# Kernel optimization log

Measured on AMD Instinct MI355X. Metric: run time of the kernel, lower is better.

## Reference

```python
import jax, jax.numpy as jnp
import numpy as np

B, S = 16, 8192
Q_DIM, K_DIM, ATTN_DIM = 512, 512, 512


def setup_inputs() -> dict:
    key = jax.random.key(0)
    k1, k2, k3, k4, k5, k6 = jax.random.split(key, 6)
    query = jax.random.normal(k1, (B, Q_DIM), dtype=jnp.float32)
    keys = jax.random.normal(k2, (B, S, K_DIM), dtype=jnp.float32)
    mask = jax.random.randint(k3, (B, S), 0, 2, dtype=jnp.int32)
    # learned params (torch Linear stores weight as [out, in]; we keep [in, out])
    Wq = jax.random.normal(k4, (Q_DIM, ATTN_DIM), dtype=jnp.float32) / np.sqrt(Q_DIM)
    Wk = jax.random.normal(k5, (K_DIM, ATTN_DIM), dtype=jnp.float32) / np.sqrt(K_DIM)
    v = jax.random.normal(k6, (ATTN_DIM,), dtype=jnp.float32) / np.sqrt(ATTN_DIM)
    return {"query": query, "keys": keys, "mask": mask, "Wq": Wq, "Wk": Wk, "v": v}


def reference(query, keys, mask, Wq, Wk, v):
    # q: [B, 1, A], k: [B, S, A]
    q = (query @ Wq)[:, None, :]
    k = jnp.einsum('bsk,ka->bsa', keys, Wk)
    # scores e: [B, S]  (v-projection reduces attn dim)
    e = jnp.einsum('bsa,a->bs', jnp.tanh(q + k), v)
    neg_min = jnp.finfo(e.dtype).min
    e = jnp.where(mask == 0, neg_min, e)
    a = jax.nn.softmax(e, axis=-1)  # [B, S]
    c = jnp.einsum('bs,bsk->bk', a, keys)  # context [B, K_DIM]
    return (c, a)
```

## Files before the change

### kernel.cpp

```cpp
#include <hip/hip_runtime.h>

#define BB 16
#define SS 8192
#define DD 512

typedef float  f32x4  __attribute__((ext_vector_type(4)));
typedef __bf16 bf16x8 __attribute__((ext_vector_type(8)));
typedef __bf16 bf16x4 __attribute__((ext_vector_type(4)));

__device__ __forceinline__ void gload_lds16(const unsigned short* g, unsigned short* l) {
    __builtin_amdgcn_global_load_lds(
        (const __attribute__((address_space(1))) unsigned int*)(g),
        (__attribute__((address_space(3))) unsigned int*)(l), 16, 0, 0);
}

__device__ __forceinline__ void cvt_store_bf4(unsigned short* dst, f32x4 v) {
    bf16x4 o;
    o.x = (__bf16)v.x; o.y = (__bf16)v.y; o.z = (__bf16)v.z; o.w = (__bf16)v.w;
    *(bf16x4*)dst = o;
}

__device__ __forceinline__ float tanh_fast(float x) {
    float e2 = __expf(2.0f * x);
    return 1.0f - 2.0f / (e2 + 1.0f);
}

__global__ void prep_kernel(const float* __restrict__ query, const float* __restrict__ Wq,
                            const float* __restrict__ Wk, float* __restrict__ qproj,
                            unsigned short* __restrict__ WkT)
{
    const int bid = blockIdx.x, t = threadIdx.x;
    if (bid < DD) {
        const int n = bid;
        for (int k = t; k < DD; k += 256) {
            __bf16 h = (__bf16)Wk[k * DD + n];
            WkT[n * DD + k] = __builtin_bit_cast(unsigned short, h);
        }
    } else {
        const int idx = (bid - DD) * 256 + t;
        const int b = idx >> 9;
        const int n = idx & 511;
        const float* q  = query + b * DD;
        const float* wp = Wq + n;
        float acc = 0.0f;
#pragma unroll 8
        for (int k = 0; k < DD; ++k)
            acc = fmaf(q[k], wp[(size_t)k * DD], acc);
        qproj[b * DD + n] = acc;
    }
}

__global__ __launch_bounds__(256, 2) void fused_kernel(
    const float* __restrict__ keys, const unsigned short* __restrict__ WkT,
    const float* __restrict__ qproj, const float* __restrict__ vvec,
    const int* __restrict__ mask, float* __restrict__ e_ws,
    float* __restrict__ cpart, float2* __restrict__ ml_ws)
{
    __shared__ unsigned short ksA[2][4 * 512];
    __shared__ unsigned short wtB[2][32 * 512];
    __shared__ float sm_part[4][64];
    __shared__ float w_sh[64];
    __shared__ f32x4 red[128];

    const int tid  = threadIdx.x;
    const int w    = tid >> 6;
    const int lane = tid & 63;
    const int ml   = lane & 15;
    const int quad = lane >> 4;
    const int bid  = blockIdx.x;
    const int b    = bid >> 7;
    const int chunk = bid & 127;
    const int s0   = chunk << 6;

    const int m  = tid >> 2;
    const int q4 = tid & 3;
    const float* krow = keys + ((size_t)(b * SS + s0 + m)) * DD + q4 * 4;
    const int it  = m >> 4;
    const int g0  = q4 >> 1;
    const int j0  = (q4 & 1) * 4;
    const int stA0 = it * 512 + ((m & 15) + 16 * g0)       * 8 + j0;
    const int stA1 = it * 512 + ((m & 15) + 16 * (g0 + 2)) * 8 + j0;

    const unsigned short* wg = WkT + (size_t)(w * 128 + ml) * DD + quad * 8;

    f32x4 acc[4][8];
#pragma unroll
    for (int i = 0; i < 4; ++i)
#pragma unroll
        for (int jn = 0; jn < 8; ++jn) acc[i][jn] = (f32x4){0.f, 0.f, 0.f, 0.f};

#pragma unroll
    for (int r = 0; r < 8; ++r)
        gload_lds16(wg + (size_t)r * 16 * DD, &wtB[0][(w * 8 + r) * 512]);
    {
        f32x4 k0 = *(const f32x4*)(krow);
        f32x4 k1 = *(const f32x4*)(krow + 16);
        cvt_store_bf4(&ksA[0][stA0], k0);
        cvt_store_bf4(&ksA[0][stA1], k1);
    }
    __syncthreads();

    for (int j = 0; j < 16; ++j) {
        const int cur = j & 1;
        const int nxt = cur ^ 1;
        f32x4 k0, k1;
        if (j < 15) {
            const int kb = (j + 1) * 32;
#pragma unroll
            for (int r = 0; r < 8; ++r)
                gload_lds16(wg + kb + (size_t)r * 16 * DD, &wtB[nxt][(w * 8 + r) * 512]);
            k0 = *(const f32x4*)(krow + kb);
            k1 = *(const f32x4*)(krow + kb + 16);
        }
        bf16x8 af[4];
#pragma unroll
        for (int i = 0; i < 4; ++i)
            af[i] = *(const bf16x8*)&ksA[cur][i * 512 + lane * 8];
#pragma unroll
        for (int jn = 0; jn < 8; ++jn) {
            bf16x8 bfr = *(const bf16x8*)&wtB[cur][(w * 8 + jn) * 512 + lane * 8];
#pragma unroll
            for (int i = 0; i < 4; ++i)
                acc[i][jn] = __builtin_amdgcn_mfma_f32_16x16x32_bf16(af[i], bfr, acc[i][jn], 0, 0, 0);
        }
        if (j < 15) {
            cvt_store_bf4(&ksA[nxt][stA0], k0);
            cvt_store_bf4(&ksA[nxt][stA1], k1);
        }
        __syncthreads();
    }

    float qv[8], vv[8];
#pragma unroll
    for (int jn = 0; jn < 8; ++jn) {
        const int n = w * 128 + jn * 16 + ml;
        qv[jn] = qproj[b * DD + n];
        vv[jn] = vvec[n];
    }
#pragma unroll
    for (int i = 0; i < 4; ++i) {
#pragma unroll
        for (int r = 0; r < 4; ++r) {
            float s = 0.0f;
#pragma unroll
            for (int jn = 0; jn < 8; ++jn) {
                float xx = acc[i][jn][r] + qv[jn];
                s += tanh_fast(xx) * vv[jn];
            }
            s += __shfl_xor(s, 1, 64);
            s += __shfl_xor(s, 2, 64);
            s += __shfl_xor(s, 4, 64);
            s += __shfl_xor(s, 8, 64);
            if (ml == 0) sm_part[w][i * 16 + quad * 4 + r] = s;
        }
    }
    __syncthreads();

    if (tid < 64) {
        float e = sm_part[0][tid] + sm_part[1][tid] + sm_part[2][tid] + sm_part[3][tid];
        const int mk = mask[b * SS + s0 + tid];
        if (mk == 0) e = -3.402823466e38f;
        e_ws[(size_t)b * SS + s0 + tid] = e;
        float mx = e;
#pragma unroll
        for (int off = 32; off >= 1; off >>= 1) mx = fmaxf(mx, __shfl_xor(mx, off, 64));
        float wv = (mk == 0) ? 0.0f : __expf(e - mx);
        float l  = wv;
#pragma unroll
        for (int off = 32; off >= 1; off >>= 1) l += __shfl_xor(l, off, 64);
        w_sh[tid] = wv;
        if (tid == 0) ml_ws[b * 128 + chunk] = make_float2(mx, l);
    }
    __syncthreads();

    const int n4 = (tid & 127) << 2;
    const int sh = tid >> 7;
    const float* kctx = keys + ((size_t)(b * SS + s0 + sh * 32)) * DD + n4;
    f32x4 cacc = (f32x4){0.f, 0.f, 0.f, 0.f};
#pragma unroll 8
    for (int sI = 0; sI < 32; ++sI) {
        float wgt = w_sh[sh * 32 + sI];
        f32x4 kv  = *(const f32x4*)(kctx + (size_t)sI * DD);
        cacc += kv * wgt;
    }
    if (sh == 1) red[tid & 127] = cacc;
    __syncthreads();
    if (sh == 0) {
        cacc += red[tid];
        *(f32x4*)(cpart + ((size_t)(b * 128 + chunk)) * 512 + n4) = cacc;
    }
}

__global__ __launch_bounds__(256) void finalize_kernel(
    const float* __restrict__ e_ws, const float* __restrict__ cpart,
    const float2* __restrict__ ml_ws, float* __restrict__ out)
{
    const int bid = blockIdx.x, t = threadIdx.x;
    const int b = (bid < 16) ? bid : ((bid - 16) >> 3);

    float mi = -3.402823466e38f, li = 0.0f;
    if (t < 128) { float2 p = ml_ws[b * 128 + t]; mi = p.x; li = p.y; }
    float mr = mi;
#pragma unroll
    for (int off = 32; off >= 1; off >>= 1) mr = fmaxf(mr, __shfl_xor(mr, off, 64));
    __shared__ float rm[4], rs[4];
    if ((t & 63) == 0) rm[t >> 6] = mr;
    __syncthreads();
    const float M = fmaxf(fmaxf(rm[0], rm[1]), fmaxf(rm[2], rm[3]));
    float si = (t < 128) ? li * __expf(mi - M) : 0.0f;
#pragma unroll
    for (int off = 32; off >= 1; off >>= 1) si += __shfl_xor(si, off, 64);
    if ((t & 63) == 0) rs[t >> 6] = si;
    __syncthreads();
    const float L = rs[0] + rs[1] + rs[2] + rs[3];
    const float invL = 1.0f / L;

    if (bid < 16) {
        const int n0 = t * 2;
        float a0 = 0.0f, a1 = 0.0f;
        for (int i = 0; i < 128; ++i) {
            float2 p = ml_ws[b * 128 + i];
            float sc = __expf(p.x - M);
            const float* cp = cpart + ((size_t)(b * 128 + i)) * 512 + n0;
            a0 = fmaf(cp[0], sc, a0);
            a1 = fmaf(cp[1], sc, a1);
        }
        out[b * DD + n0]     = a0 * invL;
        out[b * DD + n0 + 1] = a1 * invL;
    } else {
        const int chunk8 = (bid - 16) & 7;
        const float* ep = e_ws + (size_t)b * SS + chunk8 * 1024;
        float* ap = out + BB * DD + (size_t)b * SS + chunk8 * 1024;
#pragma unroll
        for (int r = 0; r < 4; ++r) {
            float e = ep[t + 256 * r];
            ap[t + 256 * r] = __expf(e - M) * invL;
        }
    }
}

extern "C" void kernel_launch(void* const* d_in, const int* in_sizes, int n_in,
                              void* d_out, int out_size, void* d_ws, size_t ws_size,
                              hipStream_t stream)
{
    const float* query = (const float*)d_in[0];
    const float* keys  = (const float*)d_in[1];
    const int*   mask  = (const int*)  d_in[2];
    const float* Wq    = (const float*)d_in[3];
    const float* Wk    = (const float*)d_in[4];
    const float* v     = (const float*)d_in[5];
    float* out = (float*)d_out;

    float*          qproj = (float*)d_ws;
    unsigned short* WkT   = (unsigned short*)((char*)d_ws + 32768);
    float*          e_ws  = (float*)((char*)d_ws + 32768 + 524288);
    float*          cpart = (float*)((char*)d_ws + 32768 + 2 * 524288);
    float2*         ml_ws = (float2*)((char*)d_ws + 32768 + 2 * 524288 + 4194304);

    prep_kernel    <<<DD + 32, 256, 0, stream>>>(query, Wq, Wk, qproj, WkT);
    fused_kernel   <<<BB * (SS / 64), 256, 0, stream>>>(keys, WkT, qproj, v, mask,
                                                        e_ws, cpart, ml_ws);
    finalize_kernel<<<16 + 128, 256, 0, stream>>>(e_ws, cpart, ml_ws, out);
}
```

Measured before the change: 547.9 us.

## Stage full key tile in LDS upfront and read Wk fragments directly from global

```diff
diff --git a/kernel.cpp b/kernel.cpp
--- a/kernel.cpp
+++ b/kernel.cpp
@@ -7,12 +7,6 @@
 typedef float  f32x4  __attribute__((ext_vector_type(4)));
 typedef __bf16 bf16x8 __attribute__((ext_vector_type(8)));
 typedef __bf16 bf16x4 __attribute__((ext_vector_type(4)));
-
-__device__ __forceinline__ void gload_lds16(const unsigned short* g, unsigned short* l) {
-    __builtin_amdgcn_global_load_lds(
-        (const __attribute__((address_space(1))) unsigned int*)(g),
-        (__attribute__((address_space(3))) unsigned int*)(l), 16, 0, 0);
-}
 
 __device__ __forceinline__ void cvt_store_bf4(unsigned short* dst, f32x4 v) {
     bf16x4 o;
@@ -56,8 +50,7 @@
     const int* __restrict__ mask, float* __restrict__ e_ws,
     float* __restrict__ cpart, float2* __restrict__ ml_ws)
 {
-    __shared__ unsigned short ksA[2][4 * 512];
-    __shared__ unsigned short wtB[2][32 * 512];
+    __shared__ unsigned short ksA[16 * 2048];
     __shared__ float sm_part[4][64];
     __shared__ float w_sh[64];
     __shared__ f32x4 red[128];
@@ -78,10 +71,18 @@
     const int it  = m >> 4;
     const int g0  = q4 >> 1;
     const int j0  = (q4 & 1) * 4;
-    const int stA0 = it * 512 + ((m & 15) + 16 * g0)       * 8 + j0;
-    const int stA1 = it * 512 + ((m & 15) + 16 * (g0 + 2)) * 8 + j0;
-
-    const unsigned short* wg = WkT + (size_t)(w * 128 + ml) * DD + quad * 8;
+    const int base0 = it * 512 + ((m & 15) + 16 * g0)       * 8 + j0;
+    const int base1 = it * 512 + ((m & 15) + 16 * (g0 + 2)) * 8 + j0;
+#pragma unroll 4
+    for (int j = 0; j < 16; ++j) {
+        f32x4 k0 = *(const f32x4*)(krow + j * 32);
+        f32x4 k1 = *(const f32x4*)(krow + j * 32 + 16);
+        cvt_store_bf4(&ksA[j * 2048 + base0], k0);
+        cvt_store_bf4(&ksA[j * 2048 + base1], k1);
+    }
+    __syncthreads();
+
+    const unsigned short* wb = WkT + (size_t)(w * 128 + ml) * DD + quad * 8;
 
     f32x4 acc[4][8];
 #pragma unroll
@@ -89,45 +90,19 @@
 #pragma unroll
         for (int jn = 0; jn < 8; ++jn) acc[i][jn] = (f32x4){0.f, 0.f, 0.f, 0.f};
 
-#pragma unroll
-    for (int r = 0; r < 8; ++r)
-        gload_lds16(wg + (size_t)r * 16 * DD, &wtB[0][(w * 8 + r) * 512]);
-    {
-        f32x4 k0 = *(const f32x4*)(krow);
-        f32x4 k1 = *(const f32x4*)(krow + 16);
-        cvt_store_bf4(&ksA[0][stA0], k0);
-        cvt_store_bf4(&ksA[0][stA1], k1);
-    }
-    __syncthreads();
-
+#pragma unroll 2
     for (int j = 0; j < 16; ++j) {
-        const int cur = j & 1;
-        const int nxt = cur ^ 1;
-        f32x4 k0, k1;
-        if (j < 15) {
-            const int kb = (j + 1) * 32;
-#pragma unroll
-            for (int r = 0; r < 8; ++r)
-                gload_lds16(wg + kb + (size_t)r * 16 * DD, &wtB[nxt][(w * 8 + r) * 512]);
-            k0 = *(const f32x4*)(krow + kb);
-            k1 = *(const f32x4*)(krow + kb + 16);
-        }
         bf16x8 af[4];
 #pragma unroll
         for (int i = 0; i < 4; ++i)
-            af[i] = *(const bf16x8*)&ksA[cur][i * 512 + lane * 8];
+            af[i] = *(const bf16x8*)&ksA[j * 2048 + (i * 64 + lane) * 8];
 #pragma unroll
         for (int jn = 0; jn < 8; ++jn) {
-            bf16x8 bfr = *(const bf16x8*)&wtB[cur][(w * 8 + jn) * 512 + lane * 8];
+            bf16x8 bfr = *(const bf16x8*)(wb + (size_t)jn * 16 * DD + j * 32);
 #pragma unroll
             for (int i = 0; i < 4; ++i)
                 acc[i][jn] = __builtin_amdgcn_mfma_f32_16x16x32_bf16(af[i], bfr, acc[i][jn], 0, 0, 0);
         }
-        if (j < 15) {
-            cvt_store_bf4(&ksA[nxt][stA0], k0);
-            cvt_store_bf4(&ksA[nxt][stA1], k1);
-        }
-        __syncthreads();
     }
 
     float qv[8], vv[8];
@@ -195,6 +170,8 @@
     const float* __restrict__ e_ws, const float* __restrict__ cpart,
     const float2* __restrict__ ml_ws, float* __restrict__ out)
 {
+    __shared__ float rm[4], rs[4];
+    __shared__ float sc_sh[128];
     const int bid = blockIdx.x, t = threadIdx.x;
     const int b = (bid < 16) ? bid : ((bid - 16) >> 3);
 
@@ -203,7 +180,6 @@
     float mr = mi;
 #pragma unroll
     for (int off = 32; off >= 1; off >>= 1) mr = fmaxf(mr, __shfl_xor(mr, off, 64));
-    __shared__ float rm[4], rs[4];
     if ((t & 63) == 0) rm[t >> 6] = mr;
     __syncthreads();
     const float M = fmaxf(fmaxf(rm[0], rm[1]), fmaxf(rm[2], rm[3]));
@@ -216,11 +192,13 @@
     const float invL = 1.0f / L;
 
     if (bid < 16) {
+        if (t < 128) sc_sh[t] = __expf(ml_ws[b * 128 + t].x - M);
+        __syncthreads();
         const int n0 = t * 2;
         float a0 = 0.0f, a1 = 0.0f;
+#pragma unroll 4
         for (int i = 0; i < 128; ++i) {
-            float2 p = ml_ws[b * 128 + i];
-            float sc = __expf(p.x - M);
+            const float sc = sc_sh[i];
             const float* cp = cpart + ((size_t)(b * 128 + i)) * 512 + n0;
             a0 = fmaf(cp[0], sc, a0);
             a1 = fmaf(cp[1], sc, a1);
```

Measured after the change: 560.4 us. +2.3%, slower.
